# Kernel optimization log

Hardware: AMD Instinct MI355X
Metric: run time of the kernel (lower is better)

The kernel has to match this reference:

```python
import jax, jax.numpy as jnp
import numpy as np

P = 4        # number of GPU partitions (hardcoded in source)
N = 65536    # nodes per partition (src = dst for diagonal blocks)
D = 128      # in_d
O = 128      # out
E = 500000   # edges per (src, dest) block
M = 32768    # unique remote dest nodes per off-diagonal block


def setup_inputs() -> dict:
    key = jax.random.key(0)
    k0, k1, k2, k3, k4, k5 = jax.random.split(key, 6)
    feats = jax.random.normal(k0, (P, N, D), dtype=jnp.float32)
    scale = np.float32(1.0 / np.sqrt(D))
    W_self = jax.random.normal(k1, (P, D, O), dtype=jnp.float32) * scale
    W_neigh = jax.random.normal(k2, (P, D, O), dtype=jnp.float32) * scale
    b = jnp.zeros((P, O), dtype=jnp.float32)
    edge_src = jax.random.randint(k3, (P, P, E), 0, N, dtype=jnp.int32)
    # dest indices: < N on the diagonal, < M off-diagonal
    dst_max = np.where(np.eye(P, dtype=bool), N, M).astype(np.int32)  # [P,P]
    edge_dst = jax.random.randint(k4, (P, P, E), 0, N, dtype=jnp.int32) % jnp.asarray(dst_max)[:, :, None]
    # unique merge indices per off-diagonal block (diagonal entries unused)
    merge_idx = jnp.stack([
        jnp.stack([
            jax.random.permutation(jax.random.fold_in(k5, s * P + d), N)[:M].astype(jnp.int32)
            for d in range(P)])
        for s in range(P)])  # [P,P,M]
    return {"feats": feats, "W_self": W_self, "W_neigh": W_neigh, "b": b,
            "edge_src": edge_src, "edge_dst": edge_dst, "merge_idx": merge_idx}


def _sage_block(feat_src, Ws, Wn, bias, e_src, e_dst, num_dst):
    # DGL SAGEConv, aggregator='mean', norm=None, bipartite block:
    #   h_neigh[v] = mean_{(u,v) in E} feat_src[u]   (0 if in-degree 0)
    #   out = feat_dst @ W_self + h_neigh @ W_neigh + b, feat_dst = feat_src[:num_dst]
    msg = feat_src[e_src]                                              # [E, D] gather
    agg = jax.ops.segment_sum(msg, e_dst, num_segments=num_dst)        # [num_dst, D]
    deg = jax.ops.segment_sum(jnp.ones((e_src.shape[0],), feat_src.dtype),
                              e_dst, num_segments=num_dst)
    h_neigh = agg / jnp.maximum(deg, 1.0)[:, None]
    return feat_src[:num_dst] @ Ws + h_neigh @ Wn + bias


def reference(feats, W_self, W_neigh, b, edge_src, edge_dst, merge_idx):
    # per-(src,dest) SAGEConv using src partition's layer weights
    outs = [[_sage_block(feats[s], W_self[s], W_neigh[s], b[s],
                         edge_src[s, d], edge_dst[s, d],
                         N if s == d else M)
             for d in range(P)] for s in range(P)]
    # cross-partition merge: final[merge_idx] += remote partial
    finals = []
    for d in range(P):
        f = outs[d][d]                                                 # [N, O]
        for s in range(P):
            if s != d:
                f = f.at[merge_idx[s, d]].add(outs[s][d])              # scatter-add [M,O]
        finals.append(f)
    return jnp.stack(finals)                                           # [P, N, O]
```

## Files before the change

### kernel.cpp

```cpp
#include <hip/hip_runtime.h>
#include <stdint.h>

#define PN 4
#define NN 65536
#define DD 128
#define OO 128
#define EE 500000
#define MM 32768
#define NW 245

typedef __attribute__((ext_vector_type(8))) short short8;
typedef __attribute__((ext_vector_type(4))) float floatx4;
typedef __attribute__((ext_vector_type(4))) float f4v;
typedef __attribute__((ext_vector_type(2))) unsigned u2v;

__device__ __forceinline__ unsigned short f2bf(float f) {
  unsigned u = __float_as_uint(f);
  u += 0x7fffu + ((u >> 16) & 1u);
  return (unsigned short)(u >> 16);
}
__device__ __forceinline__ float bfhi2f(unsigned u) { return __uint_as_float(u & 0xffff0000u); }
__device__ __forceinline__ float bflo2f(unsigned u) { return __uint_as_float(u << 16); }

__device__ __forceinline__ long rowbase(int b) {
  int diagb = (b + 4) / 5;
  int offb = b - diagb;
  return (long)diagb * NN + (long)offb * MM;
}
__device__ __forceinline__ int offidx(int b) { return b - (b + 4) / 5; }

__global__ __launch_bounds__(256) void cvt_kernel(const float* __restrict__ f,
                                                  unsigned short* __restrict__ o) {
  size_t i = (size_t)blockIdx.x * blockDim.x + threadIdx.x;
  f4v v = __builtin_nontemporal_load((const f4v*)f + i);
  uint2 r;
  r.x = ((unsigned)f2bf(v[1]) << 16) | f2bf(v[0]);
  r.y = ((unsigned)f2bf(v[3]) << 16) | f2bf(v[2]);
  ((uint2*)o)[i] = r;
}

__global__ __launch_bounds__(256) void packW_kernel(const float* __restrict__ Ws,
                                                    const float* __restrict__ Wn,
                                                    unsigned short* __restrict__ Wp) {
  int i = blockIdx.x * 256 + threadIdx.x;
  int k = i & 127;
  int col = (i >> 7) & 127;
  int s = (i >> 14) & 3;
  int mat = i >> 16;
  const float* W = mat ? Wn : Ws;
  Wp[i] = f2bf(W[((size_t)s * DD + k) * OO + col]);
}

__global__ __launch_bounds__(256) void bucket_count(const int* __restrict__ edst,
                                                    int* __restrict__ mat) {
  __shared__ int hist[256];
  int b = blockIdx.y, w = blockIdx.x, t = threadIdx.x;
  hist[t] = 0;
  __syncthreads();
  size_t ebase = (size_t)b * EE;
#pragma unroll
  for (int k = 0; k < 8; ++k) {
    int e = w * 2048 + k * 256 + t;
    if (e < EE) atomicAdd(&hist[edst[ebase + e] >> 8], 1);
  }
  __syncthreads();
  mat[((size_t)b * NW + w) * 256 + t] = hist[t];
}

__global__ __launch_bounds__(256) void bucket_colscan(int* __restrict__ mat,
                                                      int* __restrict__ btot) {
  int t = threadIdx.x;
  int wid = blockIdx.x * 4 + (t >> 6);
  int l = t & 63;
  int b = wid >> 8, beta = wid & 255;
  int run = 0;
  for (int c = 0; c < 4; ++c) {
    int w = c * 64 + l;
    size_t idx = ((size_t)b * NW + w) * 256 + beta;
    int v = (w < NW) ? mat[idx] : 0;
    int x = v;
#pragma unroll
    for (int off = 1; off < 64; off <<= 1) {
      int y = __shfl_up(x, off);
      if (l >= off) x += y;
    }
    if (w < NW) mat[idx] = run + x - v;
    run += __shfl(x, 63);
  }
  if (l == 0) btot[b * 256 + beta] = run;
}

__global__ __launch_bounds__(256) void bucket_base(const int* __restrict__ btot,
                                                   int* __restrict__ bbase) {
  __shared__ int sc[256];
  int b = blockIdx.x, t = threadIdx.x;
  int v = btot[b * 256 + t];
  sc[t] = v;
  __syncthreads();
  for (int off = 1; off < 256; off <<= 1) {
    int x = (t >= off) ? sc[t - off] : 0;
    __syncthreads();
    sc[t] += x;
    __syncthreads();
  }
  bbase[b * 256 + t] = sc[t] - v;
}

__global__ __launch_bounds__(256) void bucket_scatter(const int* __restrict__ esrc,
                                                      const int* __restrict__ edst,
                                                      const int* __restrict__ mat,
                                                      const int* __restrict__ bbase,
                                                      uint2* __restrict__ tmp) {
  __shared__ int cur[256];
  int b = blockIdx.y, w = blockIdx.x, t = threadIdx.x;
  cur[t] = bbase[b * 256 + t] + mat[((size_t)b * NW + w) * 256 + t];
  __syncthreads();
  size_t ebase = (size_t)b * EE;
#pragma unroll
  for (int k = 0; k < 8; ++k) {
    int e = w * 2048 + k * 256 + t;
    if (e < EE) {
      int dv = __builtin_nontemporal_load(&edst[ebase + e]);
      int sv = __builtin_nontemporal_load(&esrc[ebase + e]);
      int p = atomicAdd(&cur[dv >> 8], 1);
      tmp[ebase + p] = (uint2){(unsigned)dv, (unsigned)sv};
    }
  }
}

__global__ __launch_bounds__(256) void csr_build(const uint2* __restrict__ tmp,
                                                 const int* __restrict__ btot,
                                                 const int* __restrict__ bbase,
                                                 int* __restrict__ deg,
                                                 int* __restrict__ offs,
                                                 int* __restrict__ csr) {
  __shared__ int hist[256], sc[256], cur[256];
  int b = blockIdx.y, beta = blockIdx.x, t = threadIdx.x;
  int cnt = btot[b * 256 + beta];
  int segbase = bbase[b * 256 + beta];
  hist[t] = 0;
  __syncthreads();
  size_t tbase = (size_t)b * EE + segbase;
  for (int i = t; i < cnt; i += 256) atomicAdd(&hist[tmp[tbase + i].x & 255], 1);
  __syncthreads();
  sc[t] = hist[t];
  __syncthreads();
  for (int off = 1; off < 256; off <<= 1) {
    int x = (t >= off) ? sc[t - off] : 0;
    __syncthreads();
    sc[t] += x;
    __syncthreads();
  }
  int excl = sc[t] - hist[t];
  int v = beta * 256 + t;
  deg[b * NN + v] = hist[t];
  offs[b * NN + v] = segbase + excl;
  cur[t] = excl;
  __syncthreads();
  const u2v* tp = (const u2v*)tmp;
  for (int i = t; i < cnt; i += 256) {
    u2v pr = __builtin_nontemporal_load(tp + tbase + i);
    int p = atomicAdd(&cur[pr[0] & 255], 1);
    csr[(size_t)b * EE + segbase + p] = (int)pr[1];
  }
}

__global__ __launch_bounds__(256) void agg_kernel(const unsigned short* __restrict__ featsbf,
                                                  const int* __restrict__ csr,
                                                  const int* __restrict__ offs,
                                                  const int* __restrict__ deg,
                                                  unsigned short* __restrict__ hbuf) {
  int b = blockIdx.y;
  int s = b >> 2, d = b & 3;
  int num_dst = (s == d) ? NN : MM;
  int v = blockIdx.x * 4 + (threadIdx.x >> 6);
  if (v >= num_dst) return;
  int l = threadIdx.x & 63;
  const unsigned* F = (const unsigned*)(featsbf + (size_t)s * NN * DD);
  int o  = __builtin_amdgcn_readfirstlane(offs[b * NN + v]);
  int dg = __builtin_amdgcn_readfirstlane(deg[b * NN + v]);
  const int* cs = csr + (size_t)b * EE + o;

  float alo[4] = {0.f, 0.f, 0.f, 0.f};
  float ahi[4] = {0.f, 0.f, 0.f, 0.f};

  for (int base = 0; base < dg; base += 64) {
    int rem = dg - base;
    int cnt = rem < 64 ? rem : 64;
    int myidx = (l < cnt) ? cs[base + l] : 0;
    int j = 0;
    for (; j + 8 <= cnt; j += 8) {
      unsigned p[8];
#pragma unroll
      for (int q = 0; q < 8; ++q) {
        int idx = __builtin_amdgcn_readlane(myidx, j + q);
        p[q] = F[(size_t)idx * 64 + l];
      }
#pragma unroll
      for (int q = 0; q < 8; ++q) { alo[q & 3] += bflo2f(p[q]); ahi[q & 3] += bfhi2f(p[q]); }
    }
    for (; j + 4 <= cnt; j += 4) {
      unsigned p[4];
#pragma unroll
      for (int q = 0; q < 4; ++q) {
        int idx = __builtin_amdgcn_readlane(myidx, j + q);
        p[q] = F[(size_t)idx * 64 + l];
      }
#pragma unroll
      for (int q = 0; q < 4; ++q) { alo[q] += bflo2f(p[q]); ahi[q] += bfhi2f(p[q]); }
    }
    for (; j < cnt; ++j) {
      int idx = __builtin_amdgcn_readlane(myidx, j);
      unsigned p = F[(size_t)idx * 64 + l];
      alo[0] += bflo2f(p); ahi[0] += bfhi2f(p);
    }
  }

  float a0 = (alo[0] + alo[1]) + (alo[2] + alo[3]);
  float a1 = (ahi[0] + ahi[1]) + (ahi[2] + ahi[3]);
  float inv = 1.0f / (float)(dg > 0 ? dg : 1);
  a0 *= inv; a1 *= inv;
  unsigned pk = ((unsigned)f2bf(a1) << 16) | f2bf(a0);
  ((unsigned*)hbuf)[(rowbase(b) + v) * 64 + l] = pk;
}

__global__ __launch_bounds__(256) void inv_zero(int* __restrict__ inv) {
  inv[blockIdx.x * 256 + threadIdx.x] = 0;
}
__global__ __launch_bounds__(256) void inv_scatter(const int* __restrict__ merge,
                                                   int* __restrict__ inv) {
  int i = blockIdx.x * 256 + threadIdx.x;
  int p = i >> 15;
  int m = i & (MM - 1);
  int s = p / 3;
  int dd = p % 3;
  int d = dd + (dd >= s ? 1 : 0);
  int u = merge[((size_t)(s * PN + d)) * MM + m];
  inv[p * NN + u] = m + 1;
}

__global__ __launch_bounds__(256) void gemm_kernel(const unsigned short* __restrict__ featsbf,
                                                   const unsigned short* __restrict__ hbuf,
                                                   const unsigned short* __restrict__ Wpack,
                                                   const float* __restrict__ bias,
                                                   const int* __restrict__ inv,
                                                   float* __restrict__ out) {
  int w = threadIdx.x >> 6;
  int l = threadIdx.x & 63;
  int d = blockIdx.y;
  int row0 = blockIdx.x * 64;
  int kq = l >> 4;
  int m16 = l & 15;
  int n0 = w * 32;

  floatx4 acc[4][2];
#pragma unroll
  for (int rt = 0; rt < 4; ++rt)
#pragma unroll
    for (int t = 0; t < 2; ++t) acc[rt][t] = (floatx4){0.f, 0.f, 0.f, 0.f};

  {
    int b = 5 * d;
    const unsigned short* Aself = featsbf + (size_t)d * NN * DD;
    const unsigned short* Ah = hbuf + (size_t)rowbase(b) * DD;
    short8 bfrag[2][4][2];
#pragma unroll
    for (int mat = 0; mat < 2; ++mat) {
      const unsigned short* WT = Wpack + ((size_t)(mat * PN + d) * OO) * DD;
#pragma unroll
      for (int kk = 0; kk < 4; ++kk)
#pragma unroll
        for (int t = 0; t < 2; ++t) {
          int col = n0 + 16 * t + m16;
          bfrag[mat][kk][t] =
              *reinterpret_cast<const short8*>(WT + (size_t)col * DD + kk * 32 + kq * 8);
        }
    }
#pragma unroll
    for (int mat = 0; mat < 2; ++mat) {
      const unsigned short* A = mat ? Ah : Aself;
#pragma unroll
      for (int kk = 0; kk < 4; ++kk)
#pragma unroll
        for (int rt = 0; rt < 4; ++rt) {
          int row = row0 + rt * 16 + m16;
          short8 af = *reinterpret_cast<const short8*>(A + (size_t)row * DD + kk * 32 + kq * 8);
          acc[rt][0] = __builtin_amdgcn_mfma_f32_16x16x32_bf16(af, bfrag[mat][kk][0], acc[rt][0], 0, 0, 0);
          acc[rt][1] = __builtin_amdgcn_mfma_f32_16x16x32_bf16(af, bfrag[mat][kk][1], acc[rt][1], 0, 0, 0);
        }
    }
  }

  int invj[3][4];
  float bj0[3], bj1[3];
#pragma unroll
  for (int j = 0; j < 3; ++j) {
    int s = j + (j >= d ? 1 : 0);
    int b = s * 4 + d;
    int p = offidx(b);
    const int* invp = inv + (size_t)p * NN;
#pragma unroll
    for (int rt = 0; rt < 4; ++rt) invj[j][rt] = invp[row0 + rt * 16 + m16];
    bj0[j] = bias[s * OO + n0 + m16];
    bj1[j] = bias[s * OO + n0 + 16 + m16];

    const unsigned short* As = featsbf + (size_t)s * NN * DD;
    const unsigned short* Hs = hbuf + (size_t)rowbase(b) * DD;
    short8 bfrag[2][4][2];
#pragma unroll
    for (int mat = 0; mat < 2; ++mat) {
      const unsigned short* WT = Wpack + ((size_t)(mat * PN + s) * OO) * DD;
#pragma unroll
      for (int kk = 0; kk < 4; ++kk)
#pragma unroll
        for (int t = 0; t < 2; ++t) {
          int col = n0 + 16 * t + m16;
          bfrag[mat][kk][t] =
              *reinterpret_cast<const short8*>(WT + (size_t)col * DD + kk * 32 + kq * 8);
        }
    }
#pragma unroll
    for (int mat = 0; mat < 2; ++mat) {
      const unsigned short* A = mat ? Hs : As;
#pragma unroll
      for (int kk = 0; kk < 4; ++kk)
#pragma unroll
        for (int rt = 0; rt < 4; ++rt) {
          int idx = invj[j][rt];
          short8 af = (short8){0, 0, 0, 0, 0, 0, 0, 0};
          if (idx > 0)
            af = *reinterpret_cast<const short8*>(A + (size_t)(idx - 1) * DD + kk * 32 + kq * 8);
          acc[rt][0] = __builtin_amdgcn_mfma_f32_16x16x32_bf16(af, bfrag[mat][kk][0], acc[rt][0], 0, 0, 0);
          acc[rt][1] = __builtin_amdgcn_mfma_f32_16x16x32_bf16(af, bfrag[mat][kk][1], acc[rt][1], 0, 0, 0);
        }
    }
  }

  float bs0 = bias[d * OO + n0 + m16];
  float bs1 = bias[d * OO + n0 + 16 + m16];
  float* outd = out + (size_t)d * NN * OO;
#pragma unroll
  for (int rt = 0; rt < 4; ++rt) {
#pragma unroll
    for (int r = 0; r < 4; ++r) {
      int row = row0 + rt * 16 + kq * 4 + r;
      float v0 = acc[rt][0][r] + bs0;
      float v1 = acc[rt][1][r] + bs1;
#pragma unroll
      for (int j = 0; j < 3; ++j) {
        int iv = __shfl(invj[j][rt], kq * 4 + r);
        if (iv > 0) { v0 += bj0[j]; v1 += bj1[j]; }
      }
      outd[(size_t)row * OO + n0 + m16] = v0;
      outd[(size_t)row * OO + n0 + 16 + m16] = v1;
    }
  }
}

extern "C" void kernel_launch(void* const* d_in, const int* in_sizes, int n_in,
                              void* d_out, int out_size, void* d_ws, size_t ws_size,
                              hipStream_t stream) {
  const float* feats = (const float*)d_in[0];
  const float* Wself = (const float*)d_in[1];
  const float* Wneigh = (const float*)d_in[2];
  const float* bias = (const float*)d_in[3];
  const int* esrc = (const int*)d_in[4];
  const int* edst = (const int*)d_in[5];
  const int* merge = (const int*)d_in[6];
  float* out = (float*)d_out;

  char* ws = (char*)d_ws;
  unsigned short* featsbf = (unsigned short*)(ws);
  int* deg   = (int*)(ws + 67108864);
  int* offs  = (int*)(ws + 71303168);
  int* csr   = (int*)(ws + 75497472);
  unsigned short* hbuf = (unsigned short*)(ws + 107497472);
  unsigned short* Wpack = (unsigned short*)(ws + 275269632);
  int* btot  = (int*)(ws + 275531776);
  int* bbase = (int*)(ws + 275548160);
  uint2* tmp = (uint2*)(ws + 107497472);
  int* mat   = (int*)(ws + 107497472 + 64000000);
  int* inv   = (int*)(ws + 75497472);

  cvt_kernel<<<(PN * NN * DD) / 4 / 256, 256, 0, stream>>>(feats, featsbf);
  packW_kernel<<<512, 256, 0, stream>>>(Wself, Wneigh, Wpack);
  bucket_count<<<dim3(NW, 16), 256, 0, stream>>>(edst, mat);
  bucket_colscan<<<1024, 256, 0, stream>>>(mat, btot);
  bucket_base<<<16, 256, 0, stream>>>(btot, bbase);
  bucket_scatter<<<dim3(NW, 16), 256, 0, stream>>>(esrc, edst, mat, bbase, tmp);
  csr_build<<<dim3(256, 16), 256, 0, stream>>>(tmp, btot, bbase, deg, offs, csr);
  agg_kernel<<<dim3(NN / 4, 16), 256, 0, stream>>>(featsbf, csr, offs, deg, hbuf);
  inv_zero<<<12 * NN / 256, 256, 0, stream>>>(inv);
  inv_scatter<<<12 * MM / 256, 256, 0, stream>>>(merge, inv);
  gemm_kernel<<<dim3(NN / 64, 4), 256, 0, stream>>>(featsbf, hbuf, Wpack, bias, inv, out);
}
```

Before: 1.101 ms.

## Stage gathered remote A/H rows into swizzled LDS shared across waves

In the GEMM merge phase, each of the four waves previously gathered the same remote feature and h rows from global memory independently, once per wave and column tile. Now the block cooperatively loads each gathered 64-row tile once, one row per wave-lane iteration with coalesced 256-byte reads. It writes the tile into XOR-swizzled shared memory and reads MFMA fragments from there. This cuts redundant global gather traffic by about 4x, at the cost of 32KB of LDS, two barriers per source partition, and possible loss of occupancy.

```diff
diff --git a/kernel.cpp b/kernel.cpp
--- a/kernel.cpp
+++ b/kernel.cpp
@@ -245,8 +245,11 @@
                                                    const float* __restrict__ bias,
                                                    const int* __restrict__ inv,
                                                    float* __restrict__ out) {
-  int w = threadIdx.x >> 6;
-  int l = threadIdx.x & 63;
+  __shared__ unsigned short Abuf[64 * 128];
+  __shared__ unsigned short Hbuf[64 * 128];
+  int tid = threadIdx.x;
+  int w = __builtin_amdgcn_readfirstlane(tid >> 6);
+  int l = tid & 63;
   int d = blockIdx.y;
   int row0 = blockIdx.x * 64;
   int kq = l >> 4;
@@ -291,21 +294,40 @@
     }
   }
 
-  int invj[3][4];
+  int ivvj[3];
   float bj0[3], bj1[3];
 #pragma unroll
   for (int j = 0; j < 3; ++j) {
     int s = j + (j >= d ? 1 : 0);
     int b = s * 4 + d;
-    int p = offidx(b);
-    const int* invp = inv + (size_t)p * NN;
-#pragma unroll
-    for (int rt = 0; rt < 4; ++rt) invj[j][rt] = invp[row0 + rt * 16 + m16];
+    const int* invp = inv + (size_t)offidx(b) * NN;
+    int ivv = invp[row0 + l];
+    ivvj[j] = ivv;
     bj0[j] = bias[s * OO + n0 + m16];
     bj1[j] = bias[s * OO + n0 + 16 + m16];
 
-    const unsigned short* As = featsbf + (size_t)s * NN * DD;
-    const unsigned short* Hs = hbuf + (size_t)rowbase(b) * DD;
+    const unsigned* Fs = (const unsigned*)(featsbf + (size_t)s * NN * DD);
+    const unsigned* Hs = (const unsigned*)(hbuf + (size_t)rowbase(b) * DD);
+
+    unsigned av[16], hv[16];
+    int ivr[16];
+#pragma unroll
+    for (int i = 0; i < 16; ++i) {
+      int iv = __builtin_amdgcn_readlane(ivv, w * 16 + i);
+      ivr[i] = iv;
+      int m = iv > 0 ? iv - 1 : 0;
+      av[i] = Fs[(size_t)m * 64 + l];
+      hv[i] = Hs[(size_t)m * 64 + l];
+    }
+#pragma unroll
+    for (int i = 0; i < 16; ++i) {
+      int r = w * 16 + i;
+      int di = r * 64 + (l ^ ((r & 7) << 2));
+      ((unsigned*)Abuf)[di] = ivr[i] > 0 ? av[i] : 0u;
+      ((unsigned*)Hbuf)[di] = ivr[i] > 0 ? hv[i] : 0u;
+    }
+    __syncthreads();
+
     short8 bfrag[2][4][2];
 #pragma unroll
     for (int mat = 0; mat < 2; ++mat) {
@@ -321,19 +343,19 @@
     }
 #pragma unroll
     for (int mat = 0; mat < 2; ++mat) {
-      const unsigned short* A = mat ? Hs : As;
+      const unsigned short* Lb = mat ? Hbuf : Abuf;
 #pragma unroll
       for (int kk = 0; kk < 4; ++kk)
 #pragma unroll
         for (int rt = 0; rt < 4; ++rt) {
-          int idx = invj[j][rt];
-          short8 af = (short8){0, 0, 0, 0, 0, 0, 0, 0};
-          if (idx > 0)
-            af = *reinterpret_cast<const short8*>(A + (size_t)(idx - 1) * DD + kk * 32 + kq * 8);
+          int row = rt * 16 + m16;
+          int boff = ((kk * 64 + kq * 16) ^ ((row & 7) << 4)) >> 1;
+          short8 af = *reinterpret_cast<const short8*>(&Lb[row * 128 + boff]);
           acc[rt][0] = __builtin_amdgcn_mfma_f32_16x16x32_bf16(af, bfrag[mat][kk][0], acc[rt][0], 0, 0, 0);
           acc[rt][1] = __builtin_amdgcn_mfma_f32_16x16x32_bf16(af, bfrag[mat][kk][1], acc[rt][1], 0, 0, 0);
         }
     }
+    __syncthreads();
   }
 
   float bs0 = bias[d * OO + n0 + m16];
@@ -348,7 +370,7 @@
       float v1 = acc[rt][1][r] + bs1;
 #pragma unroll
       for (int j = 0; j < 3; ++j) {
-        int iv = __shfl(invj[j][rt], kq * 4 + r);
+        int iv = __shfl(ivvj[j], rt * 16 + kq * 4 + r);
         if (iv > 0) { v0 += bj0[j]; v1 += bj1[j]; }
       }
       outd[(size_t)row * OO + n0 + m16] = v0;
```

Measured after the change: 932.6 us. 15.3% less time.
